# Performance work log

Hardware: AMD Instinct MI355X
Metric: run time of the kernel (lower is better)

Reference implementation:

```python
import jax, jax.numpy as jnp
import numpy as np

B, T1, T2, NFEAT, H = 8, 512, 1500, 1024, 16
DK = NFEAT // H


def setup_inputs() -> dict:
    key = jax.random.key(0)
    ks = jax.random.split(key, 8)
    s = 0.02
    return {
        "x": jax.random.normal(ks[0], (B, T1, NFEAT), dtype=jnp.float32),
        "memory": jax.random.normal(ks[1], (B, T2, NFEAT), dtype=jnp.float32),
        "memory_mask": jnp.ones((B, 1, T2), dtype=jnp.int32),
        "Wq": jax.random.normal(ks[2], (NFEAT, NFEAT), dtype=jnp.float32) * s,
        "bq": jnp.zeros((NFEAT,), dtype=jnp.float32),
        "Wkv": jax.random.normal(ks[3], (NFEAT, 2 * NFEAT), dtype=jnp.float32) * s,
        "bkv": jnp.zeros((2 * NFEAT,), dtype=jnp.float32),
        "Wout": jax.random.normal(ks[4], (NFEAT, NFEAT), dtype=jnp.float32) * s,
        "bout": jnp.zeros((NFEAT,), dtype=jnp.float32),
    }


def reference(x, memory, memory_mask, Wq, bq, Wkv, bkv, Wout, bout):
    b, t1, _ = x.shape
    t2 = memory.shape[1]
    # projections (W stored as (in, out))
    q = x @ Wq + bq                                   # (b, t1, n_feat)
    kv = memory @ Wkv + bkv                           # (b, t2, 2*n_feat)
    k, v = jnp.split(kv, 2, axis=-1)
    q_h = q.reshape(b, t1, H, DK).transpose(0, 2, 1, 3)   # (b,h,t1,dk)
    k_h = k.reshape(b, t2, H, DK).transpose(0, 2, 1, 3)   # (b,h,t2,dk)
    v_h = v.reshape(b, t2, H, DK).transpose(0, 2, 1, 3)   # (b,h,t2,dk)
    q_h = q_h * (DK ** -0.5)
    scores = jnp.einsum("bhqd,bhkd->bhqk", q_h, k_h)      # (b,h,t1,t2)
    mask0 = (memory_mask[:, None, :, :] == 0)             # (b,1,1 or t1,t2)
    scores = jnp.where(mask0, -jnp.inf, scores)
    attn = jax.nn.softmax(scores, axis=-1)
    attn = jnp.where(mask0, 0.0, attn)
    ctx = jnp.einsum("bhqk,bhkd->bhqd", attn, v_h)        # (b,h,t1,dk)
    ctx = ctx.transpose(0, 2, 1, 3).reshape(b, t1, H * DK)
    return ctx @ Wout + bout
```

## Files before the change

kernel.cpp:

```cpp
#include <hip/hip_runtime.h>
#include <cstdint>
#include <cstddef>

typedef __attribute__((ext_vector_type(8))) short short8;
typedef __attribute__((ext_vector_type(4))) float f32x4;

__device__ __forceinline__ unsigned short bf16_rne(float f) {
  unsigned int u = __float_as_uint(f);
  u += 0x7FFFu + ((u >> 16) & 1u);
  return (unsigned short)(u >> 16);
}

__global__ void __launch_bounds__(256) k_cvt(const float* __restrict__ in,
                                             unsigned short* __restrict__ out, int n8) {
  int i = blockIdx.x * 256 + threadIdx.x;
  if (i >= n8) return;
  float4 a = reinterpret_cast<const float4*>(in)[2 * i];
  float4 b = reinterpret_cast<const float4*>(in)[2 * i + 1];
  short8 v;
  v[0] = (short)bf16_rne(a.x); v[1] = (short)bf16_rne(a.y);
  v[2] = (short)bf16_rne(a.z); v[3] = (short)bf16_rne(a.w);
  v[4] = (short)bf16_rne(b.x); v[5] = (short)bf16_rne(b.y);
  v[6] = (short)bf16_rne(b.z); v[7] = (short)bf16_rne(b.w);
  reinterpret_cast<short8*>(out)[i] = v;
}

__global__ void __launch_bounds__(256) k_tcvt(const float* __restrict__ W,
                                              unsigned short* __restrict__ WT,
                                              int R, int C) {
  __shared__ float t[64][65];
  const int c0 = blockIdx.x * 64, r0 = blockIdx.y * 64;
  const int lr = threadIdx.x >> 6, lc = threadIdx.x & 63;
#pragma unroll
  for (int i = 0; i < 16; ++i)
    t[i * 4 + lr][lc] = W[(size_t)(r0 + i * 4 + lr) * C + c0 + lc];
  __syncthreads();
#pragma unroll
  for (int i = 0; i < 16; ++i) {
    int ro = i * 4 + lr;
    WT[(size_t)(c0 + ro) * R + r0 + lc] = bf16_rne(t[lc][ro]);
  }
}

__global__ void __launch_bounds__(256) k_pad(unsigned short* __restrict__ pk,
                                             unsigned short* __restrict__ pv) {
  int i = blockIdx.x * 256 + threadIdx.x;
  if (i >= 128 * 36 * 64) return;
  int head = i / (36 * 64);
  int rem = i - head * (36 * 64);
  int t2 = rem / 64 + 1500;
  int dk = rem & 63;
  size_t ik = ((size_t)(head * 24 + 23) * 8 + (dk >> 3)) * 512 + (t2 & 63) * 8 + (dk & 7);
  size_t iv = ((size_t)(head * 24 + 23) * 8 + ((t2 >> 3) & 7)) * 512 + dk * 8 + (t2 & 7);
  pk[ik] = 0;
  pv[iv] = 0;
}

template <int MODE>
__global__ void __launch_bounds__(256) k_gemm(const unsigned short* __restrict__ A,
                                              const unsigned short* __restrict__ BT,
                                              const float* __restrict__ bias,
                                              void* __restrict__ out1,
                                              void* __restrict__ out2,
                                              int M, int K) {
  __shared__ unsigned short As[128 * 64];
  __shared__ unsigned short Bs[128 * 64];
  const int tid = threadIdx.x;
  const int lane = tid & 63;
  const int wid = tid >> 6;
  const int grp = lane >> 4, lm = lane & 15;
  const int m0 = blockIdx.x * 128, n0 = blockIdx.y * 128;
  const int wm = (wid >> 1) * 64, wn = (wid & 1) * 64;
  const int srow = tid >> 3;
  const int sw = (tid & 7) * 16;

  f32x4 acc[4][4] = {};

  const int nkt = K >> 6;
  for (int kt = 0; kt < nkt; ++kt) {
    short8 va[4], vb[4];
#pragma unroll
    for (int c = 0; c < 4; ++c) {
      int row = c * 32 + srow;
      int ra = m0 + row; if (ra > M - 1) ra = M - 1;
      va[c] = *reinterpret_cast<const short8*>(A + (size_t)ra * K + kt * 64 + (sw >> 1));
      vb[c] = *reinterpret_cast<const short8*>(BT + (size_t)(n0 + row) * K + kt * 64 + (sw >> 1));
    }
    __syncthreads();
#pragma unroll
    for (int c = 0; c < 4; ++c) {
      int row = c * 32 + srow;
      int dst = row * 64 + ((sw ^ ((row & 7) << 4)) >> 1);
      *reinterpret_cast<short8*>(&As[dst]) = va[c];
      *reinterpret_cast<short8*>(&Bs[dst]) = vb[c];
    }
    __syncthreads();

    short8 af[4][2], bfr[4][2];
#pragma unroll
    for (int m = 0; m < 4; ++m)
#pragma unroll
      for (int ks = 0; ks < 2; ++ks) {
        int row = wm + m * 16 + lm;
        int off = (ks * 64 + grp * 16) ^ ((row & 7) << 4);
        af[m][ks] = *reinterpret_cast<const short8*>(&As[row * 64 + (off >> 1)]);
      }
#pragma unroll
    for (int n = 0; n < 4; ++n)
#pragma unroll
      for (int ks = 0; ks < 2; ++ks) {
        int row = wn + n * 16 + lm;
        int off = (ks * 64 + grp * 16) ^ ((row & 7) << 4);
        bfr[n][ks] = *reinterpret_cast<const short8*>(&Bs[row * 64 + (off >> 1)]);
      }
#pragma unroll
    for (int m = 0; m < 4; ++m)
#pragma unroll
      for (int n = 0; n < 4; ++n)
#pragma unroll
        for (int ks = 0; ks < 2; ++ks)
          acc[m][n] = __builtin_amdgcn_mfma_f32_16x16x32_bf16(af[m][ks], bfr[n][ks],
                                                              acc[m][n], 0, 0, 0);
  }

#pragma unroll
  for (int m = 0; m < 4; ++m) {
    int rbase = m0 + wm + m * 16 + grp * 4;
#pragma unroll
    for (int n = 0; n < 4; ++n) {
      int cg = n0 + wn + n * 16 + lm;
      float bs = bias[cg];
#pragma unroll
      for (int r = 0; r < 4; ++r) {
        int row = rbase + r;
        float v = acc[m][n][r] + bs;
        if (MODE == 0) {
          v *= 0.180336884f;
          int b = row >> 9, t1 = row & 511, h = cg >> 6, dk = cg & 63;
          ((unsigned short*)out1)[(((size_t)b * 16 + h) * 512 + t1) * 64 + dk] = bf16_rne(v);
        } else if (MODE == 1) {
          if (row < M) {
            int b = row / 1500, t2 = row - b * 1500;
            if (cg < 1024) {
              int h = cg >> 6, dk = cg & 63;
              int head = b * 16 + h;
              size_t idx = ((size_t)(head * 24 + (t2 >> 6)) * 8 + (dk >> 3)) * 512 +
                           (t2 & 63) * 8 + (dk & 7);
              ((unsigned short*)out1)[idx] = bf16_rne(v);
            } else {
              int h = (cg - 1024) >> 6, dk = (cg - 1024) & 63;
              int head = b * 16 + h;
              size_t idx = ((size_t)(head * 24 + (t2 >> 6)) * 8 + ((t2 >> 3) & 7)) * 512 +
                           dk * 8 + (t2 & 7);
              ((unsigned short*)out2)[idx] = bf16_rne(v);
            }
          }
        } else {
          ((float*)out1)[(size_t)row * 1024 + cg] = v;
        }
      }
    }
  }
}

__global__ void __launch_bounds__(256) k_attn(const unsigned short* __restrict__ Q,
                                              const unsigned short* __restrict__ PK,
                                              const unsigned short* __restrict__ PV,
                                              const int* __restrict__ mask,
                                              float* __restrict__ po,
                                              float* __restrict__ dn) {
  __shared__ unsigned short Ps[4][16 * 64];
  const int tid = threadIdx.x, lane = tid & 63, wid = tid >> 6;
  const int grp = lane >> 4, lm = lane & 15;
  const int bid = blockIdx.x;
  const int logical = (bid & 7) * 256 + (bid >> 3);
  const int head = logical >> 4, qt = (logical >> 1) & 7, half = logical & 1;
  const int b = head >> 4, h = head & 15;
  const int kt0 = half * 12;

  const unsigned short* qbase = Q + ((size_t)head * 512 + qt * 64) * 64;
  const unsigned short* kf = PK + (size_t)head * 98304 + grp * 512 + lm * 8;
  const unsigned short* vf = PV + (size_t)head * 98304 + grp * 512 + lm * 8;
  const int* mrow = mask + b * 1500;

  short8 aq[2];
#pragma unroll
  for (int ks = 0; ks < 2; ++ks)
    aq[ks] = *reinterpret_cast<const short8*>(qbase + (wid * 16 + lm) * 64 + ks * 32 + grp * 8);

  unsigned long long mlo = 0ull;
#pragma unroll
  for (int i = 0; i < 48; ++i) {
    int col = (kt0 + (i >> 2)) * 64 + (i & 3) * 16 + lm;
    unsigned int ok = (col < 1500) ? (mrow[col] != 0 ? 1u : 0u) : 0u;
    mlo |= (unsigned long long)ok << i;
  }

  f32x4 O[4] = {};
  f32x4 O4 = {0.f, 0.f, 0.f, 0.f};
  const short8 onesb = {(short)0x3F80, (short)0x3F80, (short)0x3F80, (short)0x3F80,
                        (short)0x3F80, (short)0x3F80, (short)0x3F80, (short)0x3F80};

  short8 bk[4][2];
#pragma unroll
  for (int n = 0; n < 4; ++n)
#pragma unroll
    for (int ks = 0; ks < 2; ++ks)
      bk[n][ks] = *reinterpret_cast<const short8*>(kf + (size_t)kt0 * 4096 + ks * 2048 + n * 128);

  for (int kt = kt0; kt < kt0 + 12; ++kt) {
    short8 bv[4][2];
#pragma unroll
    for (int n2 = 0; n2 < 4; ++n2)
#pragma unroll
      for (int ks = 0; ks < 2; ++ks)
        bv[n2][ks] = *reinterpret_cast<const short8*>(vf + (size_t)kt * 4096 + ks * 2048 + n2 * 128);

    f32x4 s[4];
#pragma unroll
    for (int n = 0; n < 4; ++n) {
      s[n] = f32x4{0.f, 0.f, 0.f, 0.f};
#pragma unroll
      for (int ks = 0; ks < 2; ++ks)
        s[n] = __builtin_amdgcn_mfma_f32_16x16x32_bf16(aq[ks], bk[n][ks], s[n], 0, 0, 0);
    }

    if (kt < kt0 + 11) {
#pragma unroll
      for (int n = 0; n < 4; ++n)
#pragma unroll
        for (int ks = 0; ks < 2; ++ks)
          bk[n][ks] = *reinterpret_cast<const short8*>(
              kf + (size_t)(kt + 1) * 4096 + ks * 2048 + n * 128);
    }

    unsigned int nib = (unsigned int)mlo & 15u;
    mlo >>= 4;
    float mb4[4];
#pragma unroll
    for (int n = 0; n < 4; ++n) mb4[n] = (nib >> n) & 1u ? -8.0f : -3.0e38f;
#pragma unroll
    for (int n = 0; n < 4; ++n)
#pragma unroll
      for (int r = 0; r < 4; ++r) s[n][r] = exp2f(s[n][r] + mb4[n]);

#pragma unroll
    for (int n = 0; n < 4; ++n)
#pragma unroll
      for (int r = 0; r < 4; ++r) {
        int prow = grp * 4 + r;
        int pb = (n * 16 + lm) * 2;
        Ps[wid][prow * 64 + ((pb ^ ((prow & 7) << 4)) >> 1)] = bf16_rne(s[n][r]);
      }
    short8 pa[2];
#pragma unroll
    for (int ks = 0; ks < 2; ++ks) {
      int off = (ks * 64 + grp * 16) ^ ((lm & 7) << 4);
      pa[ks] = *reinterpret_cast<const short8*>(&Ps[wid][lm * 64 + (off >> 1)]);
    }

#pragma unroll
    for (int n2 = 0; n2 < 4; ++n2)
#pragma unroll
      for (int ks = 0; ks < 2; ++ks)
        O[n2] = __builtin_amdgcn_mfma_f32_16x16x32_bf16(pa[ks], bv[n2][ks], O[n2], 0, 0, 0);
#pragma unroll
    for (int ks = 0; ks < 2; ++ks)
      O4 = __builtin_amdgcn_mfma_f32_16x16x32_bf16(pa[ks], onesb, O4, 0, 0, 0);
  }

  float* orow = po + (size_t)half * 4194304 +
                ((size_t)(b * 512 + qt * 64 + wid * 16 + grp * 4)) * 1024 + h * 64;
#pragma unroll
  for (int r = 0; r < 4; ++r)
#pragma unroll
    for (int n2 = 0; n2 < 4; ++n2)
      orow[r * 1024 + n2 * 16 + lm] = O[n2][r];
  if (lm == 0) {
    int t1g = b * 512 + qt * 64 + wid * 16 + grp * 4;
#pragma unroll
    for (int r = 0; r < 4; ++r)
      dn[half * 65536 + (t1g + r) * 16 + h] = O4[r];
  }
}

__global__ void __launch_bounds__(256) k_comb(const float* __restrict__ po,
                                              const float* __restrict__ dn,
                                              unsigned short* __restrict__ ctx) {
  int idx = blockIdx.x * 256 + threadIdx.x;
  if (idx >= 524288) return;
  int row = idx >> 7, c8 = idx & 127;
  int col0 = c8 * 8, h = c8 >> 3;
  float d = dn[row * 16 + h] + dn[65536 + row * 16 + h];
  float inv = 1.0f / d;
  const float4* p0 = reinterpret_cast<const float4*>(po + (size_t)row * 1024 + col0);
  const float4* p1 = reinterpret_cast<const float4*>(po + 4194304 + (size_t)row * 1024 + col0);
  float4 a0 = p0[0], a1 = p0[1], b0 = p1[0], b1 = p1[1];
  short8 v;
  v[0] = (short)bf16_rne((a0.x + b0.x) * inv);
  v[1] = (short)bf16_rne((a0.y + b0.y) * inv);
  v[2] = (short)bf16_rne((a0.z + b0.z) * inv);
  v[3] = (short)bf16_rne((a0.w + b0.w) * inv);
  v[4] = (short)bf16_rne((a1.x + b1.x) * inv);
  v[5] = (short)bf16_rne((a1.y + b1.y) * inv);
  v[6] = (short)bf16_rne((a1.z + b1.z) * inv);
  v[7] = (short)bf16_rne((a1.w + b1.w) * inv);
  reinterpret_cast<short8*>(ctx)[idx] = v;
}

extern "C" void kernel_launch(void* const* d_in, const int* in_sizes, int n_in,
                              void* d_out, int out_size, void* d_ws, size_t ws_size,
                              hipStream_t stream) {
  const float* x = (const float*)d_in[0];
  const float* mem = (const float*)d_in[1];
  const int* mask = (const int*)d_in[2];
  const float* Wq = (const float*)d_in[3];
  const float* bq = (const float*)d_in[4];
  const float* Wkv = (const float*)d_in[5];
  const float* bkv = (const float*)d_in[6];
  const float* Wout = (const float*)d_in[7];
  const float* bout = (const float*)d_in[8];

  uint8_t* w = (uint8_t*)d_ws;
  unsigned short* xb    = (unsigned short*)(w);
  unsigned short* mb    = (unsigned short*)(w + 8388608);
  unsigned short* wqT   = (unsigned short*)(w + 32964608);
  unsigned short* wkvT  = (unsigned short*)(w + 35061760);
  unsigned short* woutT = (unsigned short*)(w + 39256064);
  unsigned short* qb    = (unsigned short*)(w + 41353216);
  unsigned short* kb    = (unsigned short*)(w + 49741824);
  unsigned short* vtb   = (unsigned short*)(w + 74907648);
  unsigned short* ctx   = (unsigned short*)(w + 100073472);
  float* po             = (float*)(w);
  float* dn             = (float*)(w + 33554432);

  k_cvt<<<2048, 256, 0, stream>>>(x, xb, 524288);
  k_cvt<<<6000, 256, 0, stream>>>(mem, mb, 1536000);
  k_tcvt<<<dim3(16, 16), 256, 0, stream>>>(Wq, wqT, 1024, 1024);
  k_tcvt<<<dim3(32, 16), 256, 0, stream>>>(Wkv, wkvT, 1024, 2048);
  k_tcvt<<<dim3(16, 16), 256, 0, stream>>>(Wout, woutT, 1024, 1024);
  k_pad<<<1152, 256, 0, stream>>>(kb, vtb);
  k_gemm<0><<<dim3(32, 8), 256, 0, stream>>>(xb, wqT, bq, qb, nullptr, 4096, 1024);
  k_gemm<1><<<dim3(94, 16), 256, 0, stream>>>(mb, wkvT, bkv, kb, vtb, 12000, 1024);
  k_attn<<<2048, 256, 0, stream>>>(qb, kb, vtb, mask, po, dn);
  k_comb<<<2048, 256, 0, stream>>>(po, dn, ctx);
  k_gemm<2><<<dim3(32, 8), 256, 0, stream>>>(ctx, woutT, bout, d_out, nullptr, 4096, 1024);
}
```

Before: 243.6 us.

## Use direct global-to-LDS loads and XCD-aware block remapping in GEMM

Replaces the register-staged global load plus LDS store in the GEMM tile loop with global_load_lds direct-to-LDS transfers, moving the swizzle onto the source address instead of the destination. It also flattens the grid to 1D and remaps block ids so that consecutive logical tiles land on the same XCD, aiming for better L2 reuse of A/B tiles. This frees VGPRs and removes the LDS write instructions. In exchange, the loop now syncs once before issuing loads, so there is still no overlap between loading and compute.

```diff
diff --git a/kernel.cpp b/kernel.cpp
--- a/kernel.cpp
+++ b/kernel.cpp
@@ -4,6 +4,13 @@
 
 typedef __attribute__((ext_vector_type(8))) short short8;
 typedef __attribute__((ext_vector_type(4))) float f32x4;
+
+typedef __attribute__((address_space(3))) unsigned int lds_u32;
+typedef const __attribute__((address_space(1))) unsigned int glb_u32;
+
+__device__ __forceinline__ void gl_lds16(const void* g, void* l) {
+  __builtin_amdgcn_global_load_lds((glb_u32*)g, (lds_u32*)l, 16, 0, 0);
+}
 
 __device__ __forceinline__ unsigned short bf16_rne(float f) {
   unsigned int u = __float_as_uint(f);
@@ -69,30 +76,29 @@
   const int lane = tid & 63;
   const int wid = tid >> 6;
   const int grp = lane >> 4, lm = lane & 15;
-  const int m0 = blockIdx.x * 128, n0 = blockIdx.y * 128;
+
+  constexpr int NBY = (MODE == 1) ? 16 : 8;
+  constexpr int NWG = (MODE == 1) ? 94 * 16 : 32 * 8;
+  constexpr int CPX = NWG / 8;
+  const int bid = blockIdx.x;
+  const int logical = (bid & 7) * CPX + (bid >> 3);
+  const int m0 = (logical / NBY) * 128, n0 = (logical % NBY) * 128;
+
   const int wm = (wid >> 1) * 64, wn = (wid & 1) * 64;
   const int srow = tid >> 3;
-  const int sw = (tid & 7) * 16;
+  const int sx = ((tid & 7) * 16) ^ ((srow & 7) << 4);
 
   f32x4 acc[4][4] = {};
 
   const int nkt = K >> 6;
   for (int kt = 0; kt < nkt; ++kt) {
-    short8 va[4], vb[4];
+    __syncthreads();
 #pragma unroll
     for (int c = 0; c < 4; ++c) {
       int row = c * 32 + srow;
       int ra = m0 + row; if (ra > M - 1) ra = M - 1;
-      va[c] = *reinterpret_cast<const short8*>(A + (size_t)ra * K + kt * 64 + (sw >> 1));
-      vb[c] = *reinterpret_cast<const short8*>(BT + (size_t)(n0 + row) * K + kt * 64 + (sw >> 1));
-    }
-    __syncthreads();
-#pragma unroll
-    for (int c = 0; c < 4; ++c) {
-      int row = c * 32 + srow;
-      int dst = row * 64 + ((sw ^ ((row & 7) << 4)) >> 1);
-      *reinterpret_cast<short8*>(&As[dst]) = va[c];
-      *reinterpret_cast<short8*>(&Bs[dst]) = vb[c];
+      gl_lds16(A + (size_t)ra * K + kt * 64 + (sx >> 1), As + c * 2048 + tid * 8);
+      gl_lds16(BT + (size_t)(n0 + row) * K + kt * 64 + (sx >> 1), Bs + c * 2048 + tid * 8);
     }
     __syncthreads();
 
@@ -340,9 +346,9 @@
   k_tcvt<<<dim3(32, 16), 256, 0, stream>>>(Wkv, wkvT, 1024, 2048);
   k_tcvt<<<dim3(16, 16), 256, 0, stream>>>(Wout, woutT, 1024, 1024);
   k_pad<<<1152, 256, 0, stream>>>(kb, vtb);
-  k_gemm<0><<<dim3(32, 8), 256, 0, stream>>>(xb, wqT, bq, qb, nullptr, 4096, 1024);
-  k_gemm<1><<<dim3(94, 16), 256, 0, stream>>>(mb, wkvT, bkv, kb, vtb, 12000, 1024);
+  k_gemm<0><<<256, 256, 0, stream>>>(xb, wqT, bq, qb, nullptr, 4096, 1024);
+  k_gemm<1><<<1504, 256, 0, stream>>>(mb, wkvT, bkv, kb, vtb, 12000, 1024);
   k_attn<<<2048, 256, 0, stream>>>(qb, kb, vtb, mask, po, dn);
   k_comb<<<2048, 256, 0, stream>>>(po, dn, ctx);
-  k_gemm<2><<<dim3(32, 8), 256, 0, stream>>>(ctx, woutT, bout, d_out, nullptr, 4096, 1024);
-}
+  k_gemm<2><<<256, 256, 0, stream>>>(ctx, woutT, bout, d_out, nullptr, 4096, 1024);
+}
```

Measured after the change: 233.0 us. 1.05x faster.
